# Performance work log

Hardware: AMD Instinct MI355X
Metric: run time of the kernel (lower is better)

The kernel has to match this reference:

```python
import jax, jax.numpy as jnp
import numpy as np

EPS = 1e-8


def setup_inputs() -> dict:
    key = jax.random.key(0)
    k1, k2 = jax.random.split(key)
    N, D, K = 200000, 256, 64
    embeds = jax.random.normal(k1, (N, D), dtype=jnp.float32)
    init = jax.random.uniform(k2, (K, D), dtype=jnp.float32)  # torch.rand(K, n_h)
    beta = jnp.ones((1,), dtype=jnp.float32)
    return {"embeds": embeds, "init": init, "beta": beta, "num_iter": 11}


def reference(embeds, init, beta, num_iter):
    # embeds: [N, D], init: [K, D], beta: scalar temperature
    data_abs = jnp.linalg.norm(embeds, axis=1, keepdims=True)            # [N, 1]
    data_norm = embeds / jnp.maximum(data_abs, EPS)                      # [N, D]
    b = beta.reshape(())
    mu = init
    r = None
    for _ in range(num_iter):  # small fixed iteration count (default 11)
        mu_abs = jnp.linalg.norm(mu, axis=1, keepdims=True)              # [K, 1]
        mu_norm = mu / jnp.maximum(mu_abs, EPS)                          # [K, D]
        dist = data_norm @ mu_norm.T                                     # [N, K]
        r = jax.nn.softmax(b * dist, axis=1)                             # [N, K]
        cluster_r = r.sum(axis=0)                                        # [K]
        cluster_mean = r.T @ embeds                                      # [K, D]
        mu = cluster_mean / cluster_r[:, None]                           # diag(1/cluster_r) @ cluster_mean
    return mu, r
```

## Files before the change

kernel.cpp:

```cpp
#include <hip/hip_runtime.h>
#include <math.h>


#define N_ROWS 200000
#define DIM 256
#define KC 64
#define NUM_ITER 11
#define TR 64
#define NTILES (N_ROWS / TR)
#define EPSV 1e-8f
#define NB 256

typedef _Float16 half8 __attribute__((ext_vector_type(8)));
typedef _Float16 half4 __attribute__((ext_vector_type(4)));
typedef float f32x4 __attribute__((ext_vector_type(4)));

typedef __attribute__((address_space(3))) void as3_void;
typedef __attribute__((address_space(1))) void as1_void;

__device__ __forceinline__ void glds16(const void* g, void* l) {
  __builtin_amdgcn_global_load_lds((const as1_void*)g, (as3_void*)l, 16, 0, 0);
}

__device__ __forceinline__ float wave_reduce_sum(float v) {
#pragma unroll
  for (int off = 32; off > 0; off >>= 1) v += __shfl_xor(v, off, 64);
  return v;
}

__device__ __forceinline__ void barrier_lgkm_only() {
  __builtin_amdgcn_sched_barrier(0);
  asm volatile("s_waitcnt lgkmcnt(0)" ::: "memory");
  __builtin_amdgcn_s_barrier();
  __builtin_amdgcn_sched_barrier(0);
}

__device__ __forceinline__ void stage_row512_8(const _Float16* g, _Float16* l,
                                               int wid, int lane) {
#pragma unroll
  for (int ii = 0; ii < 4; ++ii) {
    int i = wid * 4 + ii;
    int row = i * 2 + (lane >> 5);
    int slot = (lane & 31) ^ (row & 7);
    glds16((const char*)g + row * 512 + slot * 16, (char*)l + i * 1024);
  }
}

__global__ __launch_bounds__(512, 1) void cluster_first(
    const float* __restrict__ embeds, const float* __restrict__ init,
    const float* __restrict__ beta, _Float16* __restrict__ Xh,
    float* __restrict__ inv_norm, float* __restrict__ part_cm,
    float* __restrict__ part_crt) {
  __shared__ alignas(16) _Float16 x_lds[2][TR * DIM];
  __shared__ alignas(16) _Float16 xt_lds[DIM * TR];
  __shared__ alignas(16) _Float16 mu_lds[KC * DIM];
  __shared__ alignas(16) _Float16 r_lds[KC * TR];
  __shared__ alignas(16) f32x4 dist_lds[16 * 64];
  __shared__ float cr_lds[4 * KC];
  __shared__ float inv_lds[TR];

  float* x32 = (float*)&x_lds[0][0];
  _Float16* xtile = xt_lds;
  _Float16* xtr = &x_lds[0][0];

  const int tid = threadIdx.x, wid = tid >> 6, lane = tid & 63;
  const int l15 = lane & 15, h = lane >> 4;
  const int kh = wid >> 2, rg = wid & 3;
  const float b = beta[0];
  const int myrow = 16 * rg + l15;
  const int rb0 = blockIdx.x;

  {
    const int cl = tid >> 3, sub = tid & 7;
    float ss = 0.f;
#pragma unroll
    for (int j = 0; j < 8; ++j) {
      float4 v = *(const float4*)(init + (size_t)cl * DIM + sub * 32 + 4 * j);
      ss = fmaf(v.x, v.x, ss); ss = fmaf(v.y, v.y, ss);
      ss = fmaf(v.z, v.z, ss); ss = fmaf(v.w, v.w, ss);
    }
    ss += __shfl_xor(ss, 1); ss += __shfl_xor(ss, 2); ss += __shfl_xor(ss, 4);
    if (sub == 0) cr_lds[cl] = ss;
  }
  __syncthreads();
  if (tid < KC) cr_lds[tid] = 1.0f / fmaxf(sqrtf(cr_lds[tid]), EPSV);
  __syncthreads();
  {
    const float4* init4 = (const float4*)init;
#pragma unroll
    for (int i = 0; i < 8; ++i) {
      const int idx = tid + 512 * i;
      const int cl = idx >> 6;
      const int dim0 = (idx & 63) * 4;
      float4 v = init4[idx];
      const float iv = cr_lds[cl];
      const int sw = dim0 ^ ((cl & 7) << 3);
      half4 hh;
      hh[0] = (_Float16)(v.x * iv); hh[1] = (_Float16)(v.y * iv);
      hh[2] = (_Float16)(v.z * iv); hh[3] = (_Float16)(v.w * iv);
      *(half4*)&mu_lds[cl * DIM + sw] = hh;
    }
  }
  __syncthreads();
  half8 amreg[4][4];
#pragma unroll
  for (int t = 0; t < 4; ++t) {
    const int kb = 128 * kh + 32 * t + 8 * h;
#pragma unroll
    for (int m = 0; m < 4; ++m) {
      const int cl = 16 * m + l15;
      amreg[t][m] = *(const half8*)&mu_lds[cl * DIM + (kb ^ ((cl & 7) << 3))];
    }
  }

  f32x4 acc2[4][2] = {};
  float cr_acc[16] = {};
  for (int rb = rb0; rb < NTILES; rb += NB) {
#pragma unroll
    for (int ii = 0; ii < 8; ++ii) {
      const int row = wid * 8 + ii;
      const int slot = lane ^ (row & 7);
      glds16((const char*)embeds + (size_t)(rb * TR + row) * 1024 + slot * 16,
             (char*)x32 + row * 1024);
    }
    __syncthreads();

    {
      const int row = tid >> 3, sub = tid & 7;
      float ss = 0.f;
      half8 hh[4];
#pragma unroll
      for (int i2 = 0; i2 < 8; ++i2) {
        const int g = sub * 8 + i2;
        float4 v = *(const float4*)((const char*)x32 + row * 1024 +
                                    ((g ^ (row & 7)) * 16));
        ss = fmaf(v.x, v.x, ss); ss = fmaf(v.y, v.y, ss);
        ss = fmaf(v.z, v.z, ss); ss = fmaf(v.w, v.w, ss);
        _Float16* hp = (_Float16*)&hh[i2 >> 1] + (i2 & 1) * 4;
        hp[0] = (_Float16)v.x; hp[1] = (_Float16)v.y;
        hp[2] = (_Float16)v.z; hp[3] = (_Float16)v.w;
      }
#pragma unroll
      for (int j = 0; j < 4; ++j) {
        const int slot = (sub * 4 + j) ^ (row & 7);
        *(half8*)((char*)xtile + row * 512 + slot * 16) = hh[j];
        *(float4*)((char*)Xh + (size_t)(rb * TR + row) * 512 + sub * 64 + j * 16) =
            *(float4*)&hh[j];
      }
      ss += __shfl_xor(ss, 1); ss += __shfl_xor(ss, 2); ss += __shfl_xor(ss, 4);
      if (sub == 0) {
        const float iv = 1.0f / fmaxf(sqrtf(ss), EPSV);
        inv_lds[row] = iv;
        inv_norm[rb * TR + row] = iv;
      }
    }
    barrier_lgkm_only();

    f32x4 acc1[4] = {};
#pragma unroll
    for (int t = 0; t < 4; ++t) {
      const int kb = 128 * kh + 32 * t + 8 * h;
      half8 bx = *(const half8*)&xtile[myrow * DIM + (kb ^ ((myrow & 7) << 3))];
#pragma unroll
      for (int m = 0; m < 4; ++m)
        acc1[m] = __builtin_amdgcn_mfma_f32_16x16x32_f16(amreg[t][m], bx, acc1[m], 0, 0, 0);
    }
    if (kh) {
#pragma unroll
      for (int m = 0; m < 4; ++m) dist_lds[(rg * 4 + m) * 64 + lane] = acc1[m];
    }
    barrier_lgkm_only();

    if (!kh) {
#pragma unroll
      for (int m = 0; m < 4; ++m) acc1[m] += dist_lds[(rg * 4 + m) * 64 + lane];
      const float sc = b * inv_lds[myrow];
#pragma unroll
      for (int m = 0; m < 4; ++m)
#pragma unroll
        for (int j = 0; j < 4; ++j) acc1[m][j] *= sc;
      float mx = -1e30f;
#pragma unroll
      for (int m = 0; m < 4; ++m)
#pragma unroll
        for (int j = 0; j < 4; ++j) mx = fmaxf(mx, acc1[m][j]);
      mx = fmaxf(mx, __shfl_xor(mx, 16));
      mx = fmaxf(mx, __shfl_xor(mx, 32));
      float esum = 0.f;
#pragma unroll
      for (int m = 0; m < 4; ++m)
#pragma unroll
        for (int j = 0; j < 4; ++j) {
          float e = __expf(acc1[m][j] - mx);
          acc1[m][j] = e;
          esum += e;
        }
      esum += __shfl_xor(esum, 16);
      esum += __shfl_xor(esum, 32);
      const float rcp = 1.0f / esum;
#pragma unroll
      for (int m = 0; m < 4; ++m)
#pragma unroll
        for (int j = 0; j < 4; ++j) {
          const float rv = acc1[m][j] * rcp;
          const int cl = 16 * m + 4 * h + j;
          cr_acc[m * 4 + j] += rv;
          r_lds[cl * TR + (myrow ^ ((cl & 7) << 3))] = (_Float16)rv;
        }
    } else {
      const int t8 = tid & 255;
      const int db = t8 >> 3, rb8 = t8 & 7;
      union U { uint4 v; unsigned u[4]; };
      U tin[8];
#pragma unroll
      for (int k2 = 0; k2 < 8; ++k2)
        tin[k2].v = *(const uint4*)&xtile[(8 * rb8 + k2) * DIM + ((8 * db) ^ (k2 << 3))];
#pragma unroll
      for (int j = 0; j < 8; ++j) {
        const unsigned sel = (j & 1) ? 0x07060302u : 0x05040100u;
        U o;
#pragma unroll
        for (int m2 = 0; m2 < 4; ++m2)
          o.u[m2] = __builtin_amdgcn_perm(tin[2 * m2 + 1].u[j >> 1],
                                          tin[2 * m2].u[j >> 1], sel);
        *(uint4*)&xtr[(8 * db + j) * TR + 8 * (rb8 ^ j)] = o.v;
      }
    }
    barrier_lgkm_only();

#pragma unroll
    for (int t = 0; t < 2; ++t) {
      const int kb = 32 * t + 8 * h;
      half8 ar[4], bx2[2];
#pragma unroll
      for (int m = 0; m < 4; ++m) {
        const int cl = 16 * m + l15;
        ar[m] = *(const half8*)&r_lds[cl * TR + (kb ^ ((cl & 7) << 3))];
      }
#pragma unroll
      for (int n = 0; n < 2; ++n) {
        const int dm = 32 * wid + 16 * n + l15;
        bx2[n] = *(const half8*)&xtr[dm * TR + (kb ^ ((dm & 7) << 3))];
      }
#pragma unroll
      for (int m = 0; m < 4; ++m)
#pragma unroll
        for (int n = 0; n < 2; ++n)
          acc2[m][n] = __builtin_amdgcn_mfma_f32_16x16x32_f16(ar[m], bx2[n], acc2[m][n], 0, 0, 0);
    }
    __syncthreads();
  }

  float* pc = part_cm + (size_t)blockIdx.x * (KC * DIM);
#pragma unroll
  for (int m = 0; m < 4; ++m)
#pragma unroll
    for (int n = 0; n < 2; ++n)
#pragma unroll
      for (int j = 0; j < 4; ++j)
        pc[(16 * m + 4 * h + j) * DIM + 32 * wid + 16 * n + l15] = acc2[m][n][j];
  if (wid < 4) {
#pragma unroll
    for (int m = 0; m < 4; ++m)
#pragma unroll
      for (int j = 0; j < 4; ++j) {
        float v = cr_acc[m * 4 + j];
        v += __shfl_xor(v, 1); v += __shfl_xor(v, 2);
        v += __shfl_xor(v, 4); v += __shfl_xor(v, 8);
        if (l15 == 0) cr_lds[wid * KC + 16 * m + 4 * h + j] = v;
      }
  }
  __syncthreads();
  if (wid == 0)
    part_crt[(size_t)lane * NB + blockIdx.x] =
        cr_lds[lane] + cr_lds[KC + lane] + cr_lds[2 * KC + lane] + cr_lds[3 * KC + lane];
}

template <int LAST>
__global__ __launch_bounds__(512, 2) void cluster_main8(
    const _Float16* __restrict__ Xh, const float* __restrict__ inv_norm,
    const float* __restrict__ beta, const float* __restrict__ mu_raw,
    const float* __restrict__ mu_ssq, float* __restrict__ part_cm,
    float* __restrict__ part_crt, float* __restrict__ r_out) {
  __shared__ alignas(16) _Float16 mu_lds[KC * DIM];
  __shared__ alignas(16) _Float16 x_lds[2][TR * DIM];
  __shared__ alignas(16) _Float16 xt_lds[DIM * TR];
  __shared__ alignas(16) _Float16 r_lds[KC * TR];
  __shared__ alignas(16) f32x4 dist_lds[16 * 64];
  __shared__ float cr_lds[4 * KC];

  const int tid = threadIdx.x, wid = tid >> 6, lane = tid & 63;
  const int l15 = lane & 15, h = lane >> 4;
  const int kh = wid >> 2, rg = wid & 3;
  const float b = beta[0];
  const int myrow = 16 * rg + l15;
  const int rb0 = blockIdx.x;

  stage_row512_8(Xh + (size_t)rb0 * TR * DIM, x_lds[0], wid, lane);

  if (tid < KC) {
    const float4 s4 = *(const float4*)&mu_ssq[4 * tid];
    cr_lds[tid] = 1.0f / fmaxf(sqrtf(s4.x + s4.y + s4.z + s4.w), EPSV);
  }
  __syncthreads();
  {
    const float4* mu_raw4 = (const float4*)mu_raw;
#pragma unroll
    for (int i = 0; i < 8; ++i) {
      const int idx = tid + 512 * i;
      const int cl = idx >> 6;
      const int dim0 = (idx & 63) * 4;
      float4 v = mu_raw4[idx];
      const float iv = cr_lds[cl];
      const int sw = dim0 ^ ((cl & 7) << 3);
      half4 hh;
      hh[0] = (_Float16)(v.x * iv); hh[1] = (_Float16)(v.y * iv);
      hh[2] = (_Float16)(v.z * iv); hh[3] = (_Float16)(v.w * iv);
      *(half4*)&mu_lds[cl * DIM + sw] = hh;
    }
  }
  __syncthreads();

  half8 amreg[4][4];
#pragma unroll
  for (int t = 0; t < 4; ++t) {
    const int kb = 128 * kh + 32 * t + 8 * h;
#pragma unroll
    for (int m = 0; m < 4; ++m) {
      const int cl = 16 * m + l15;
      amreg[t][m] = *(const half8*)&mu_lds[cl * DIM + (kb ^ ((cl & 7) << 3))];
    }
  }

  f32x4 acc2[4][2] = {};
  float cr_acc[16] = {};
  int p = 0;
  for (int rb = rb0; rb < NTILES; rb += NB, p ^= 1) {
    const int row0 = rb * TR;
    const int rbn = rb + NB;
    if (rbn < NTILES)
      stage_row512_8(Xh + (size_t)rbn * TR * DIM, x_lds[p ^ 1], wid, lane);

    f32x4 acc1[4] = {};
    const _Float16* xb = x_lds[p];
#pragma unroll
    for (int t = 0; t < 4; ++t) {
      const int kb = 128 * kh + 32 * t + 8 * h;
      half8 bx = *(const half8*)&xb[myrow * DIM + (kb ^ ((myrow & 7) << 3))];
#pragma unroll
      for (int m = 0; m < 4; ++m)
        acc1[m] = __builtin_amdgcn_mfma_f32_16x16x32_f16(amreg[t][m], bx, acc1[m], 0, 0, 0);
    }
    if (kh) {
#pragma unroll
      for (int m = 0; m < 4; ++m) dist_lds[(rg * 4 + m) * 64 + lane] = acc1[m];
    }
    barrier_lgkm_only();

    if (!kh) {
#pragma unroll
      for (int m = 0; m < 4; ++m) acc1[m] += dist_lds[(rg * 4 + m) * 64 + lane];
      const int xr = row0 + myrow;
      const float sc = b * inv_norm[xr];
#pragma unroll
      for (int m = 0; m < 4; ++m)
#pragma unroll
        for (int j = 0; j < 4; ++j) acc1[m][j] *= sc;
      float mx = -1e30f;
#pragma unroll
      for (int m = 0; m < 4; ++m)
#pragma unroll
        for (int j = 0; j < 4; ++j) mx = fmaxf(mx, acc1[m][j]);
      mx = fmaxf(mx, __shfl_xor(mx, 16));
      mx = fmaxf(mx, __shfl_xor(mx, 32));
      float esum = 0.f;
#pragma unroll
      for (int m = 0; m < 4; ++m)
#pragma unroll
        for (int j = 0; j < 4; ++j) {
          float e = __expf(acc1[m][j] - mx);
          acc1[m][j] = e;
          esum += e;
        }
      esum += __shfl_xor(esum, 16);
      esum += __shfl_xor(esum, 32);
      const float rcp = 1.0f / esum;
#pragma unroll
      for (int m = 0; m < 4; ++m) {
#pragma unroll
        for (int j = 0; j < 4; ++j) {
          const float rv = acc1[m][j] * rcp;
          acc1[m][j] = rv;
          const int cl = 16 * m + 4 * h + j;
          cr_acc[m * 4 + j] += rv;
          r_lds[cl * TR + (myrow ^ ((cl & 7) << 3))] = (_Float16)rv;
        }
        if (LAST)
          *(float4*)&r_out[(size_t)xr * KC + 16 * m + 4 * h] = *(float4*)&acc1[m];
      }
    } else {
      const int t8 = tid & 255;
      const int db = t8 >> 3, rb8 = t8 & 7;
      union U { uint4 v; unsigned u[4]; };
      U tin[8];
#pragma unroll
      for (int k2 = 0; k2 < 8; ++k2)
        tin[k2].v = *(const uint4*)&xb[(8 * rb8 + k2) * DIM + ((8 * db) ^ (k2 << 3))];
#pragma unroll
      for (int j = 0; j < 8; ++j) {
        const unsigned sel = (j & 1) ? 0x07060302u : 0x05040100u;
        U o;
#pragma unroll
        for (int m2 = 0; m2 < 4; ++m2)
          o.u[m2] = __builtin_amdgcn_perm(tin[2 * m2 + 1].u[j >> 1],
                                          tin[2 * m2].u[j >> 1], sel);
        *(uint4*)&xt_lds[(8 * db + j) * TR + 8 * (rb8 ^ j)] = o.v;
      }
    }

    barrier_lgkm_only();

#pragma unroll
    for (int t = 0; t < 2; ++t) {
      const int kb = 32 * t + 8 * h;
      half8 ar[4], bx2[2];
#pragma unroll
      for (int m = 0; m < 4; ++m) {
        const int cl = 16 * m + l15;
        ar[m] = *(const half8*)&r_lds[cl * TR + (kb ^ ((cl & 7) << 3))];
      }
#pragma unroll
      for (int n = 0; n < 2; ++n) {
        const int dm = 32 * wid + 16 * n + l15;
        bx2[n] = *(const half8*)&xt_lds[dm * TR + (kb ^ ((dm & 7) << 3))];
      }
#pragma unroll
      for (int m = 0; m < 4; ++m)
#pragma unroll
        for (int n = 0; n < 2; ++n)
          acc2[m][n] = __builtin_amdgcn_mfma_f32_16x16x32_f16(ar[m], bx2[n], acc2[m][n], 0, 0, 0);
    }
    __syncthreads();
  }

  float* pc = part_cm + (size_t)blockIdx.x * (KC * DIM);
#pragma unroll
  for (int m = 0; m < 4; ++m)
#pragma unroll
    for (int n = 0; n < 2; ++n)
#pragma unroll
      for (int j = 0; j < 4; ++j)
        pc[(16 * m + 4 * h + j) * DIM + 32 * wid + 16 * n + l15] = acc2[m][n][j];
  if (wid < 4) {
#pragma unroll
    for (int m = 0; m < 4; ++m)
#pragma unroll
      for (int j = 0; j < 4; ++j) {
        float v = cr_acc[m * 4 + j];
        v += __shfl_xor(v, 1); v += __shfl_xor(v, 2);
        v += __shfl_xor(v, 4); v += __shfl_xor(v, 8);
        if (l15 == 0) cr_lds[wid * KC + 16 * m + 4 * h + j] = v;
      }
  }
  __syncthreads();
  if (wid == 0)
    part_crt[(size_t)lane * NB + blockIdx.x] =
        cr_lds[lane] + cr_lds[KC + lane] + cr_lds[2 * KC + lane] + cr_lds[3 * KC + lane];
}

template <int FINAL>
__global__ void reduce_mu(const float* __restrict__ part_cm,
                          const float* __restrict__ part_crt,
                          float* __restrict__ mu_raw, float* __restrict__ mu_ssq,
                          float* __restrict__ mu_out) {
  const int cl = blockIdx.x, q = blockIdx.y;
  const int tid = threadIdx.x, wid = tid >> 6, lane = tid & 63;
  __shared__ float red2[4 * 64];
  __shared__ float cr4[4];
  float c = part_crt[(size_t)cl * NB + tid];
  c = wave_reduce_sum(c);
  if (lane == 0) cr4[wid] = c;
  float s = 0.f;
  const float* basep =
      part_cm + (size_t)(64 * wid) * (KC * DIM) + cl * DIM + 64 * q + lane;
#pragma unroll 8
  for (int i = 0; i < 64; ++i) s += basep[(size_t)i * (KC * DIM)];
  red2[wid * 64 + lane] = s;
  __syncthreads();
  if (wid == 0) {
    const float crv = cr4[0] + cr4[1] + cr4[2] + cr4[3];
    const float st = red2[lane] + red2[64 + lane] + red2[128 + lane] + red2[192 + lane];
    const float mu = st / crv;
    const int dim = 64 * q + lane;
    if (FINAL) {
      mu_out[cl * DIM + dim] = mu;
    } else {
      mu_raw[cl * DIM + dim] = mu;
      float ss = wave_reduce_sum(mu * mu);
      if (lane == 0) mu_ssq[cl * 4 + q] = ss;
    }
  }
}

__global__ void rownorm_v1(const float* __restrict__ embeds, float* __restrict__ inv_norm) {
  int gw = (blockIdx.x * blockDim.x + threadIdx.x) >> 6;
  int lane = threadIdx.x & 63;
  int nw = (gridDim.x * blockDim.x) >> 6;
  for (int row = gw; row < N_ROWS; row += nw) {
    const float* rp = embeds + (size_t)row * DIM;
    float s = 0.f;
#pragma unroll
    for (int j = 0; j < 4; ++j) { float v = rp[lane + 64 * j]; s = fmaf(v, v, s); }
    s = wave_reduce_sum(s);
    if (lane == 0) inv_norm[row] = 1.0f / fmaxf(sqrtf(s), EPSV);
  }
}
__global__ void prep0_v1(const float* __restrict__ init, float* __restrict__ muT) {
  int k = blockIdx.x, lane = threadIdx.x;
  const float* rp = init + k * DIM;
  float v[4]; float s = 0.f;
#pragma unroll
  for (int j = 0; j < 4; ++j) { v[j] = rp[lane + 64 * j]; s = fmaf(v[j], v[j], s); }
  s = wave_reduce_sum(s);
  float inv = 1.0f / fmaxf(sqrtf(s), EPSV);
#pragma unroll
  for (int j = 0; j < 4; ++j) muT[(lane + 64 * j) * KC + k] = v[j] * inv;
}
__device__ __forceinline__ float wave_reduce_max_v1(float v) {
#pragma unroll
  for (int off = 32; off > 0; off >>= 1) v = fmaxf(v, __shfl_xor(v, off, 64));
  return v;
}
template <int LAST>
__global__ __launch_bounds__(256, 1) void main_v1(
    const float* __restrict__ embeds, const float* __restrict__ inv_norm,
    const float* __restrict__ muT, const float* __restrict__ beta,
    float* __restrict__ part_cm, float* __restrict__ part_cr,
    float* __restrict__ r_out, int nb) {
  __shared__ float mu_l[DIM * KC];
  __shared__ float x_l[TR * DIM];
  __shared__ float r_l[TR * KC];
  __shared__ float cr_l[4 * KC];
  const int tid = threadIdx.x, wid = tid >> 6, lane = tid & 63;
  const float b = beta[0];
  {
    const float4* m4 = (const float4*)muT; float4* ml4 = (float4*)mu_l;
#pragma unroll
    for (int i = 0; i < 16; ++i) ml4[tid + i * 256] = m4[tid + i * 256];
  }
  float acc[64];
#pragma unroll
  for (int i = 0; i < 64; ++i) acc[i] = 0.f;
  float cr = 0.f;
  for (int rb = blockIdx.x; rb < NTILES; rb += nb) {
    const int row0 = rb * TR;
    __syncthreads();
    {
      const float4* x4 = (const float4*)(embeds + (size_t)row0 * DIM);
      float4* xl4 = (float4*)x_l;
#pragma unroll
      for (int i = 0; i < 16; ++i) xl4[tid + i * 256] = x4[tid + i * 256];
    }
    __syncthreads();
    float dist[16];
#pragma unroll
    for (int r = 0; r < 16; ++r) dist[r] = 0.f;
    const int rbase = wid * 16;
    for (int d = 0; d < DIM; d += 4) {
      float mv0 = mu_l[(d + 0) * KC + lane], mv1 = mu_l[(d + 1) * KC + lane];
      float mv2 = mu_l[(d + 2) * KC + lane], mv3 = mu_l[(d + 3) * KC + lane];
#pragma unroll
      for (int r = 0; r < 16; ++r) {
        float4 xv = *(const float4*)&x_l[(rbase + r) * DIM + d];
        dist[r] = fmaf(xv.x, mv0, dist[r]); dist[r] = fmaf(xv.y, mv1, dist[r]);
        dist[r] = fmaf(xv.z, mv2, dist[r]); dist[r] = fmaf(xv.w, mv3, dist[r]);
      }
    }
#pragma unroll
    for (int r = 0; r < 16; ++r) {
      const int row = rbase + r;
      float s = b * (dist[r] * inv_norm[row0 + row]);
      float m = wave_reduce_max_v1(s);
      float e = __expf(s - m);
      float sum = wave_reduce_sum(e);
      float rv = e * (1.0f / sum);
      cr += rv;
      r_l[row * KC + lane] = rv;
      if (LAST) r_out[(size_t)(row0 + row) * KC + lane] = rv;
    }
    __syncthreads();
    const int dbase = wid * 64;
    for (int row = 0; row < TR; ++row) {
      float rv = r_l[row * KC + lane];
#pragma unroll
      for (int dd = 0; dd < 64; dd += 4) {
        float4 xv = *(const float4*)&x_l[row * DIM + dbase + dd];
        acc[dd + 0] = fmaf(rv, xv.x, acc[dd + 0]); acc[dd + 1] = fmaf(rv, xv.y, acc[dd + 1]);
        acc[dd + 2] = fmaf(rv, xv.z, acc[dd + 2]); acc[dd + 3] = fmaf(rv, xv.w, acc[dd + 3]);
      }
    }
  }
  {
    float* pp = part_cm + ((size_t)blockIdx.x * KC + lane) * DIM + wid * 64;
#pragma unroll
    for (int dd = 0; dd < 64; dd += 4)
      *(float4*)&pp[dd] = make_float4(acc[dd], acc[dd + 1], acc[dd + 2], acc[dd + 3]);
    cr_l[wid * KC + lane] = cr;
  }
  __syncthreads();
  if (wid == 0) {
    float c = cr_l[lane] + cr_l[64 + lane] + cr_l[128 + lane] + cr_l[192 + lane];
    part_cr[(size_t)blockIdx.x * KC + lane] = c;
  }
}
template <int FINAL>
__global__ void reduce_v1(const float* __restrict__ part_cm, const float* __restrict__ part_cr,
                          float* __restrict__ muT, float* __restrict__ mu_out, int nb) {
  const int k = blockIdx.x, t = threadIdx.x;
  __shared__ float red[256];
  float s = 0.f;
  for (int bl = 0; bl < nb; ++bl) s += part_cm[((size_t)bl * KC + k) * DIM + t];
  float c = 0.f;
  for (int bl = t; bl < nb; bl += 256) c += part_cr[(size_t)bl * KC + k];
  red[t] = c; __syncthreads();
#pragma unroll
  for (int off = 128; off > 0; off >>= 1) { if (t < off) red[t] += red[t + off]; __syncthreads(); }
  const float crv = red[0]; __syncthreads();
  const float mu = s / crv;
  if (FINAL) { mu_out[k * DIM + t] = mu; return; }
  red[t] = mu * mu; __syncthreads();
#pragma unroll
  for (int off = 128; off > 0; off >>= 1) { if (t < off) red[t] += red[t + off]; __syncthreads(); }
  const float inv = 1.0f / fmaxf(sqrtf(red[0]), EPSV);
  muT[t * KC + k] = mu * inv;
}

extern "C" void kernel_launch(void* const* d_in, const int* in_sizes, int n_in,
                              void* d_out, int out_size, void* d_ws, size_t ws_size,
                              hipStream_t stream) {
  const float* embeds = (const float*)d_in[0];
  const float* init = (const float*)d_in[1];
  const float* beta = (const float*)d_in[2];
  float* out_mu = (float*)d_out;
  float* out_r = out_mu + KC * DIM;
  char* ws = (char*)d_ws;

  const size_t szX = (size_t)N_ROWS * DIM * 2;
  const size_t szInv = (size_t)N_ROWS * 4;
  const size_t szMuR = (size_t)KC * DIM * 4;
  const size_t szSsq = (size_t)KC * 4 * 4;
  const size_t szPC = (size_t)NB * KC * DIM * 4;
  const size_t szPR = (size_t)KC * NB * 4;
  const size_t need = szX + szInv + szMuR + szSsq + szPC + szPR;

  if (ws_size >= need) {
    char* pp = ws;
    _Float16* Xh = (_Float16*)pp; pp += szX;
    float* invn = (float*)pp; pp += szInv;
    float* mu_raw = (float*)pp; pp += szMuR;
    float* mu_ssq = (float*)pp; pp += szSsq;
    float* pcm = (float*)pp; pp += szPC;
    float* pcrt = (float*)pp;

    cluster_first<<<NB, 512, 0, stream>>>(embeds, init, beta, Xh, invn, pcm, pcrt);
    for (int it = 1; it < NUM_ITER; ++it) {
      reduce_mu<0><<<dim3(KC, 4), 256, 0, stream>>>(pcm, pcrt, mu_raw, mu_ssq, nullptr);
      if (it == NUM_ITER - 1)
        cluster_main8<1><<<NB, 512, 0, stream>>>(Xh, invn, beta, mu_raw, mu_ssq,
                                                 pcm, pcrt, out_r);
      else
        cluster_main8<0><<<NB, 512, 0, stream>>>(Xh, invn, beta, mu_raw, mu_ssq,
                                                 pcm, pcrt, out_r);
    }
    reduce_mu<1><<<dim3(KC, 4), 256, 0, stream>>>(pcm, pcrt, nullptr, nullptr, out_mu);
  } else {
    float* wsf = (float*)d_ws;
    float* muT = wsf;
    float* invn = muT + DIM * KC;
    size_t avail = ws_size / sizeof(float);
    size_t fixed = (size_t)DIM * KC + N_ROWS;
    size_t per_blk = (size_t)KC * DIM + KC;
    int nb = 256;
    if (avail > fixed) {
      size_t mx = (avail - fixed) / per_blk;
      if (mx < 256) nb = (int)mx;
    } else nb = 1;
    if (nb < 1) nb = 1;
    float* pcm = invn + N_ROWS;
    float* pcr = pcm + (size_t)nb * KC * DIM;

    rownorm_v1<<<2048, 256, 0, stream>>>(embeds, invn);
    prep0_v1<<<KC, 64, 0, stream>>>(init, muT);
    for (int it = 0; it < NUM_ITER; ++it) {
      if (it > 0) reduce_v1<0><<<KC, 256, 0, stream>>>(pcm, pcr, muT, nullptr, nb);
      if (it == NUM_ITER - 1)
        main_v1<1><<<nb, 256, 0, stream>>>(embeds, invn, muT, beta, pcm, pcr, out_r, nb);
      else
        main_v1<0><<<nb, 256, 0, stream>>>(embeds, invn, muT, beta, pcm, pcr, nullptr, nb);
    }
    reduce_v1<1><<<KC, 256, 0, stream>>>(pcm, pcr, muT, out_mu, nb);
  }
}
```

Measured before the change: 490.7 us.

## Prefetch next embeds tile into LDS during compute in first-pass kernel

Moves the asynchronous global-to-LDS load of the embeds tile out of the loop head. The first tile is issued before the init normalization, and the next tile is issued right after the current one is converted to fp16, so the load overlaps the MFMA and softmax work. The transpose scratch buffer is moved onto mu_lds because x_lds now holds in-flight data. It also rotates the per-lane read and write order during the fp16 conversion to spread LDS bank and global-store accesses. This relies on later barriers in the loop body waiting for the outstanding loads, which adds a hazard risk.

```diff
diff --git a/kernel.cpp b/kernel.cpp
--- a/kernel.cpp
+++ b/kernel.cpp
@@ -61,7 +61,7 @@
 
   float* x32 = (float*)&x_lds[0][0];
   _Float16* xtile = xt_lds;
-  _Float16* xtr = &x_lds[0][0];
+  _Float16* xtr = mu_lds;
 
   const int tid = threadIdx.x, wid = tid >> 6, lane = tid & 63;
   const int l15 = lane & 15, h = lane >> 4;
@@ -70,6 +70,14 @@
   const int myrow = 16 * rg + l15;
   const int rb0 = blockIdx.x;
 
+#pragma unroll
+  for (int ii = 0; ii < 8; ++ii) {
+    const int row = wid * 8 + ii;
+    const int slot = lane ^ (row & 7);
+    glds16((const char*)embeds + (size_t)(rb0 * TR + row) * 1024 + slot * 16,
+           (char*)x32 + row * 1024);
+  }
+
   {
     const int cl = tid >> 3, sub = tid & 7;
     float ss = 0.f;
@@ -82,9 +90,9 @@
     ss += __shfl_xor(ss, 1); ss += __shfl_xor(ss, 2); ss += __shfl_xor(ss, 4);
     if (sub == 0) cr_lds[cl] = ss;
   }
-  __syncthreads();
+  barrier_lgkm_only();
   if (tid < KC) cr_lds[tid] = 1.0f / fmaxf(sqrtf(cr_lds[tid]), EPSV);
-  __syncthreads();
+  barrier_lgkm_only();
   {
     const float4* init4 = (const float4*)init;
 #pragma unroll
@@ -101,7 +109,7 @@
       *(half4*)&mu_lds[cl * DIM + sw] = hh;
     }
   }
-  __syncthreads();
+  barrier_lgkm_only();
   half8 amreg[4][4];
 #pragma unroll
   for (int t = 0; t < 4; ++t) {
@@ -112,40 +120,35 @@
       amreg[t][m] = *(const half8*)&mu_lds[cl * DIM + (kb ^ ((cl & 7) << 3))];
     }
   }
+  __syncthreads();
 
   f32x4 acc2[4][2] = {};
   float cr_acc[16] = {};
   for (int rb = rb0; rb < NTILES; rb += NB) {
-#pragma unroll
-    for (int ii = 0; ii < 8; ++ii) {
-      const int row = wid * 8 + ii;
-      const int slot = lane ^ (row & 7);
-      glds16((const char*)embeds + (size_t)(rb * TR + row) * 1024 + slot * 16,
-             (char*)x32 + row * 1024);
-    }
-    __syncthreads();
-
     {
       const int row = tid >> 3, sub = tid & 7;
       float ss = 0.f;
       half8 hh[4];
 #pragma unroll
       for (int i2 = 0; i2 < 8; ++i2) {
-        const int g = sub * 8 + i2;
+        const int q = i2 ^ sub;
+        const int g = sub * 8 + q;
         float4 v = *(const float4*)((const char*)x32 + row * 1024 +
                                     ((g ^ (row & 7)) * 16));
         ss = fmaf(v.x, v.x, ss); ss = fmaf(v.y, v.y, ss);
         ss = fmaf(v.z, v.z, ss); ss = fmaf(v.w, v.w, ss);
-        _Float16* hp = (_Float16*)&hh[i2 >> 1] + (i2 & 1) * 4;
+        _Float16* hp = (_Float16*)&hh[q >> 1] + (q & 1) * 4;
         hp[0] = (_Float16)v.x; hp[1] = (_Float16)v.y;
         hp[2] = (_Float16)v.z; hp[3] = (_Float16)v.w;
       }
 #pragma unroll
       for (int j = 0; j < 4; ++j) {
-        const int slot = (sub * 4 + j) ^ (row & 7);
-        *(half8*)((char*)xtile + row * 512 + slot * 16) = hh[j];
-        *(float4*)((char*)Xh + (size_t)(rb * TR + row) * 512 + sub * 64 + j * 16) =
-            *(float4*)&hh[j];
+        const int jj = j ^ ((sub >> 1) & 3);
+        const int g16 = sub * 4 + jj;
+        const int slot = g16 ^ (row & 7);
+        *(half8*)((char*)xtile + row * 512 + slot * 16) = hh[jj];
+        *(float4*)((char*)Xh + (size_t)(rb * TR + row) * 512 + g16 * 16) =
+            *(float4*)&hh[jj];
       }
       ss += __shfl_xor(ss, 1); ss += __shfl_xor(ss, 2); ss += __shfl_xor(ss, 4);
       if (sub == 0) {
@@ -155,6 +158,16 @@
       }
     }
     barrier_lgkm_only();
+
+    if (rb + NB < NTILES) {
+#pragma unroll
+      for (int ii = 0; ii < 8; ++ii) {
+        const int row = wid * 8 + ii;
+        const int slot = lane ^ (row & 7);
+        glds16((const char*)embeds + (size_t)((rb + NB) * TR + row) * 1024 + slot * 16,
+               (char*)x32 + row * 1024);
+      }
+    }
 
     f32x4 acc1[4] = {};
 #pragma unroll
```

Result: slower. 547.7 us (+11.6%).
